# Optimization experiments

Measured on AMD Instinct MI355X. Metric: run time of the kernel, lower is better.

## Reference

```python
import jax, jax.numpy as jnp
import numpy as np

N_TASK, N_WORKER, N_STATION = 20000, 5000, 1000
D, HEADS, LAYERS = 64, 4, 2
EDGE_COUNTS = [50000, 30000, 30000, 40000, 40000]
# (n_src, n_dst) per relation: precedes, assigned_to, has_task, can_do, done_by
EDGE_SPEC = [(N_TASK, N_TASK), (N_TASK, N_STATION), (N_STATION, N_TASK), (N_WORKER, N_TASK), (N_TASK, N_WORKER)]
EDGE_TYPES = [('task', 'task'), ('task', 'station'), ('station', 'task'), ('worker', 'task'), ('task', 'worker')]


def setup_inputs() -> dict:
    key = jax.random.key(0)
    ks = iter(jax.random.split(key, 64))
    inp = {}
    inp['x_task'] = jax.random.normal(next(ks), (N_TASK, 16), jnp.float32)
    inp['x_worker'] = jax.random.normal(next(ks), (N_WORKER, 12), jnp.float32)
    inp['x_station'] = jax.random.normal(next(ks), (N_STATION, 10), jnp.float32)
    for i, (E, (ns, nd)) in enumerate(zip(EDGE_COUNTS, EDGE_SPEC)):
        src = jax.random.randint(next(ks), (E,), 0, ns)
        dst = jax.random.randint(next(ks), (E,), 0, nd)
        inp[f'ei{i}'] = jnp.stack([src, dst]).astype(jnp.int32)
    def lin(k, i, o):
        return jax.random.normal(k, (i, o), jnp.float32) / np.float32(np.sqrt(i))
    # feature embedder params (Linear + LayerNorm affine) per node type
    for name, fd in [('task', 16), ('worker', 12), ('station', 10)]:
        inp[f'W_{name}'] = lin(next(ks), fd, D)
        inp[f'b_{name}'] = jnp.zeros((D,), jnp.float32)
        inp[f'g_{name}'] = jnp.ones((D,), jnp.float32)
        inp[f'beta_{name}'] = jnp.zeros((D,), jnp.float32)
    # stacked GATv2 params: [layers, 5 edge types, ...]
    inp['gat_Wl'] = jax.random.normal(next(ks), (LAYERS, 5, D, HEADS * D), jnp.float32) / np.float32(np.sqrt(D))
    inp['gat_Wr'] = jax.random.normal(next(ks), (LAYERS, 5, D, HEADS * D), jnp.float32) / np.float32(np.sqrt(D))
    inp['gat_att'] = jax.random.normal(next(ks), (LAYERS, 5, HEADS, D), jnp.float32) * np.float32(0.1)
    inp['gat_bias'] = jnp.zeros((LAYERS, 5, D), jnp.float32)
    return inp


def _layer_norm(x, g, b):
    m = x.mean(-1, keepdims=True)
    v = ((x - m) ** 2).mean(-1, keepdims=True)
    return (x - m) * jax.lax.rsqrt(v + 1e-5) * g + b


def _gatv2(x_src, x_dst, ei, Wl, Wr, att, bias):
    # GATv2Conv, concat=False (mean over heads), no self loops
    n_dst = x_dst.shape[0]
    xl = (x_src @ Wl).reshape(-1, HEADS, D)  # [Ns,H,Dh]
    xr = (x_dst @ Wr).reshape(-1, HEADS, D)  # [Nd,H,Dh]
    src, dst = ei[0], ei[1]
    e = jax.nn.leaky_relu(xl[src] + xr[dst], 0.2)          # [E,H,Dh]
    logits = jnp.einsum('ehd,hd->eh', e, att)              # [E,H]
    m = jax.ops.segment_max(logits, dst, num_segments=n_dst)
    ex = jnp.exp(logits - m[dst])
    denom = jax.ops.segment_sum(ex, dst, num_segments=n_dst)
    alpha = ex / denom[dst]                                # segment softmax per dst node
    out = jax.ops.segment_sum(alpha[..., None] * xl[src], dst, num_segments=n_dst)
    return out.mean(axis=1) + bias                         # [Nd,D]


def _forward(x_task, x_worker, x_station, eis,
             W_task, b_task, g_task, beta_task,
             W_worker, b_worker, g_worker, beta_worker,
             W_station, b_station, g_station, beta_station,
             gat_Wl, gat_Wr, gat_att, gat_bias):
    x = {
        'task': jax.nn.relu(_layer_norm(x_task @ W_task + b_task, g_task, beta_task)),
        'worker': jax.nn.relu(_layer_norm(x_worker @ W_worker + b_worker, g_worker, beta_worker)),
        'station': jax.nn.relu(_layer_norm(x_station @ W_station + b_station, g_station, beta_station)),
    }
    for l in range(LAYERS):
        agg = {'task': 0.0, 'worker': 0.0, 'station': 0.0}
        for t, (st, dt) in enumerate(EDGE_TYPES):
            agg[dt] = agg[dt] + _gatv2(x[st], x[dt], eis[t], gat_Wl[l, t], gat_Wr[l, t], gat_att[l, t], gat_bias[l, t])
        x = {k: jax.nn.relu(agg[k]) + x[k] for k in x}  # HeteroConv sum aggr, then ReLU + residual
    gc = jnp.concatenate([
        x['station'].mean(0), x['task'].mean(0), x['worker'].mean(0),
        x['station'].max(0), x['task'].max(0), x['worker'].max(0),
    ])[None, :]  # [1, 6*D]
    return x['task'], x['worker'], x['station'], gc


def reference(x_task, x_worker, x_station, ei0, ei1, ei2, ei3, ei4,
              W_task, b_task, g_task, beta_task,
              W_worker, b_worker, g_worker, beta_worker,
              W_station, b_station, g_station, beta_station,
              gat_Wl, gat_Wr, gat_att, gat_bias):
    return _forward(x_task, x_worker, x_station, (ei0, ei1, ei2, ei3, ei4),
                    W_task, b_task, g_task, beta_task,
                    W_worker, b_worker, g_worker, beta_worker,
                    W_station, b_station, g_station, beta_station,
                    gat_Wl, gat_Wr, gat_att, gat_bias)
```

## Files before the change

### kernel.cpp

```cpp
#include <hip/hip_runtime.h>
#include <math.h>

#define NT 20000
#define NW 5000
#define NS 1000

typedef __attribute__((ext_vector_type(8))) short bf16x8;
typedef __attribute__((ext_vector_type(4))) float f32x4;

struct GemmSeg { const short* X; const short* Wt; short* Y; int N; int blk0; };
struct GemmTab { GemmSeg s[10]; int nseg; };

struct GatSeg { const int* rowp; const int* col; const short* xl; const short* xr;
                const float* att; const float* bias; float* agg; int Nd; int wave0; };
struct GatTab { GatSeg s[5]; int nseg; };

struct EdgeSeg { const int* ei; int* cnt; int* col; int E; int blk0; };
struct EdgeTab { EdgeSeg s[5]; int nseg; };

struct ScanTab { int* cnt[5]; int* rowp[5]; int n[5]; };

__device__ __forceinline__ float wsum64(float v) {
  #pragma unroll
  for (int o = 32; o > 0; o >>= 1) v += __shfl_xor(v, o, 64);
  return v;
}
__device__ __forceinline__ short f2b(float f) {
  unsigned u = __float_as_uint(f);
  unsigned r = (u + 0x7FFFu + ((u >> 16) & 1u)) >> 16;
  return (short)(unsigned short)r;
}
__device__ __forceinline__ float blo(unsigned x) { return __uint_as_float(x << 16); }
__device__ __forceinline__ float bhi(unsigned x) { return __uint_as_float(x & 0xFFFF0000u); }

__global__ void wprep_kernel(const float* __restrict__ gWl, const float* __restrict__ gWr,
                             short* __restrict__ Wlt, short* __restrict__ Wrt,
                             int* __restrict__ nxtAll, int nZero) {
  int idx = blockIdx.x * 256 + threadIdx.x;
  if (idx < nZero) nxtAll[idx] = 0;
  int side = idx >= 163840;
  int j = idx - side * 163840;
  int m = j >> 14;
  int e = j & 16383;
  int k = e >> 8, colv = e & 255;
  const float* src = side ? gWr : gWl;
  short* dst = side ? Wrt : Wlt;
  dst[m * 16384 + colv * 64 + k] = f2b(src[m * 16384 + e]);
}

__global__ void embed_kernel(const float* __restrict__ xT, const float* __restrict__ xW,
                             const float* __restrict__ xS,
                             const float* __restrict__ WT, const float* __restrict__ WW,
                             const float* __restrict__ WS,
                             const float* __restrict__ pT, const float* __restrict__ pW,
                             const float* __restrict__ pS,
                             float* __restrict__ yT, float* __restrict__ yW,
                             float* __restrict__ yS,
                             short* __restrict__ bT, short* __restrict__ bW,
                             short* __restrict__ bS) {
  int gid  = blockIdx.x * blockDim.x + threadIdx.x;
  int wid  = gid >> 6;
  int lane = gid & 63;
  const float* x; const float* W; const float* pp; float* y; short* yb; int FD; int n;
  if (wid < NT)            { x = xT; W = WT; pp = pT; y = yT; yb = bT; FD = 16; n = wid; }
  else if (wid < NT + NW)  { x = xW; W = WW; pp = pW; y = yW; yb = bW; FD = 12; n = wid - NT; }
  else if (wid < NT + NW + NS) { x = xS; W = WS; pp = pS; y = yS; yb = bS; FD = 10; n = wid - NT - NW; }
  else return;
  const float* xr = x + (size_t)n * FD;
  float acc = pp[lane];
  for (int k = 0; k < FD; ++k) acc = fmaf(xr[k], W[k * 64 + lane], acc);
  float m = wsum64(acc) * (1.f / 64.f);
  float d = acc - m;
  float v = wsum64(d * d) * (1.f / 64.f);
  float o = d * rsqrtf(v + 1e-5f) * pp[64 + lane] + pp[128 + lane];
  o = fmaxf(o, 0.f);
  y[(size_t)n * 64 + lane] = o;
  yb[(size_t)n * 64 + lane] = f2b(o);
}

__global__ void packp_kernel(const float* b0, const float* g0, const float* be0,
                             const float* b1, const float* g1, const float* be1,
                             const float* b2, const float* g2, const float* be2,
                             float* __restrict__ out) {
  int i = threadIdx.x;
  out[i]       = b0[i];  out[64 + i]  = g0[i];  out[128 + i] = be0[i];
  out[192 + i] = b1[i];  out[256 + i] = g1[i];  out[320 + i] = be1[i];
  out[384 + i] = b2[i];  out[448 + i] = g2[i];  out[512 + i] = be2[i];
}

__global__ void count_kernel(EdgeTab tab) {
  int b = blockIdx.x, si = 0;
  for (int i = 1; i < tab.nseg; ++i) if (b >= tab.s[i].blk0) si = i;
  EdgeSeg sg = tab.s[si];
  int e = (b - sg.blk0) * 256 + threadIdx.x;
  if (e < sg.E) atomicAdd(&sg.cnt[sg.ei[sg.E + e]], 1);
}

__global__ void scan_kernel(ScanTab tab) {
  int t = blockIdx.x;
  int* cnt = tab.cnt[t]; int* rowp = tab.rowp[t]; int n = tab.n[t];
  __shared__ int wsums[16];
  __shared__ int carry_s;
  int tid = threadIdx.x, lane = tid & 63, w = tid >> 6;
  if (tid == 0) carry_s = 0;
  __syncthreads();
  for (int base = 0; base < n; base += 1024) {
    int i = base + tid;
    int v = (i < n) ? cnt[i] : 0;
    int s = v;
    #pragma unroll
    for (int o = 1; o < 64; o <<= 1) { int x = __shfl_up(s, o, 64); if (lane >= o) s += x; }
    if (lane == 63) wsums[w] = s;
    __syncthreads();
    if (w == 0 && lane < 16) {
      int x = wsums[lane];
      #pragma unroll
      for (int o = 1; o < 16; o <<= 1) { int y = __shfl_up(x, o, 16); if (lane >= o) x += y; }
      wsums[lane] = x;
    }
    __syncthreads();
    int carry   = carry_s;
    int waveoff = (w == 0) ? 0 : wsums[w - 1];
    int exc     = carry + waveoff + s - v;
    if (i < n) { rowp[i] = exc; cnt[i] = exc; }
    __syncthreads();
    if (tid == 0) carry_s += wsums[15];
    __syncthreads();
  }
  if (threadIdx.x == 0) rowp[n] = carry_s;
}

__global__ void fill_kernel(EdgeTab tab) {
  int b = blockIdx.x, si = 0;
  for (int i = 1; i < tab.nseg; ++i) if (b >= tab.s[i].blk0) si = i;
  EdgeSeg sg = tab.s[si];
  int e = (b - sg.blk0) * 256 + threadIdx.x;
  if (e >= sg.E) return;
  int s = sg.ei[e], d = sg.ei[sg.E + e];
  int pos = atomicAdd(&sg.cnt[d], 1);
  sg.col[pos] = s;
}

__global__ __launch_bounds__(256) void gemm_kernel(GemmTab tab) {
  __shared__ short lds[4096 + 16896];
  int b = blockIdx.x, si = 0;
  for (int i = 1; i < tab.nseg; ++i) if (b >= tab.s[i].blk0) si = i;
  GemmSeg sg = tab.s[si];
  int r0 = (b - sg.blk0) * 64;
  int tid = threadIdx.x;
  #pragma unroll
  for (int it = 0; it < 2; ++it) {
    int idx = it * 256 + tid;
    int row = idx >> 3, kq = idx & 7;
    bf16x8 v = {0, 0, 0, 0, 0, 0, 0, 0};
    if (r0 + row < sg.N) v = *(const bf16x8*)&sg.X[(size_t)(r0 + row) * 64 + kq * 8];
    *(bf16x8*)&lds[(row * 8 + (kq ^ (row & 7))) * 8] = v;
  }
  #pragma unroll
  for (int it = 0; it < 8; ++it) {
    int idx = it * 256 + tid;
    int col = idx >> 3, kq = idx & 7;
    bf16x8 v = *(const bf16x8*)&sg.Wt[col * 64 + kq * 8];
    *(bf16x8*)&lds[4096 + (col * 8 + (kq ^ (col & 7))) * 8] = v;
  }
  __syncthreads();
  int lane = tid & 63, wv = tid >> 6;
  int r = lane & 15, hk = lane >> 4;
  f32x4 acc[4][4];
  #pragma unroll
  for (int rt = 0; rt < 4; ++rt)
    #pragma unroll
    for (int ct = 0; ct < 4; ++ct) acc[rt][ct] = (f32x4){0.f, 0.f, 0.f, 0.f};
  #pragma unroll
  for (int kk = 0; kk < 2; ++kk) {
    int kq = kk * 4 + hk;
    bf16x8 a[4], bb[4];
    #pragma unroll
    for (int rt = 0; rt < 4; ++rt) {
      int row = rt * 16 + r;
      a[rt] = *(const bf16x8*)&lds[(row * 8 + (kq ^ (row & 7))) * 8];
    }
    #pragma unroll
    for (int ct = 0; ct < 4; ++ct) {
      int col = wv * 64 + ct * 16 + r;
      bb[ct] = *(const bf16x8*)&lds[4096 + (col * 8 + (kq ^ (col & 7))) * 8];
    }
    #pragma unroll
    for (int rt = 0; rt < 4; ++rt)
      #pragma unroll
      for (int ct = 0; ct < 4; ++ct)
        acc[rt][ct] = __builtin_amdgcn_mfma_f32_16x16x32_bf16(a[rt], bb[ct], acc[rt][ct], 0, 0, 0);
  }
  __syncthreads();
  #pragma unroll
  for (int rt = 0; rt < 4; ++rt)
    #pragma unroll
    for (int j = 0; j < 4; ++j) {
      int rowl = rt * 16 + hk * 4 + j;
      #pragma unroll
      for (int ct = 0; ct < 4; ++ct)
        lds[rowl * 264 + wv * 64 + ct * 16 + r] = f2b(acc[rt][ct][j]);
    }
  __syncthreads();
  #pragma unroll
  for (int it = 0; it < 8; ++it) {
    int idx = it * 256 + tid;
    int row = idx >> 5, v8 = idx & 31;
    if (r0 + row < sg.N) {
      bf16x8 v = *(const bf16x8*)&lds[row * 264 + v8 * 8];
      *(bf16x8*)&sg.Y[(size_t)(r0 + row) * 256 + v8 * 8] = v;
    }
  }
}

__global__ void gat_kernel(GatTab tab) {
  int gwave = (blockIdx.x * blockDim.x + threadIdx.x) >> 6;
  int lane  = threadIdx.x & 63;
  int si = 0;
  for (int i = 1; i < tab.nseg; ++i) if (gwave >= tab.s[i].wave0) si = i;
  GatSeg sg = tab.s[si];
  int n = gwave - sg.wave0;
  if (n >= sg.Nd) return;
  int h = lane >> 4, lig = lane & 15;
  uint2 xru = *(const uint2*)&sg.xr[(size_t)n * 256 + h * 64 + lig * 4];
  float4 a4 = *(const float4*)&sg.att[h * 64 + lig * 4];
  int beg = sg.rowp[n], end = sg.rowp[n + 1];
  int d = end - beg;
  float xr0 = blo(xru.x), xr1 = bhi(xru.x), xr2 = blo(xru.y), xr3 = bhi(xru.y);
  float den = 0.f, c0 = 0.f, c1 = 0.f, c2 = 0.f, c3 = 0.f;
  for (int sc = 0; sc < d; sc += 64) {
    int scn = min(64, d - sc);
    int myc = (lane < scn) ? sg.col[beg + sc + lane] : 0;
    for (int cb = 0; cb < scn; cb += 8) {
      int m = min(8, scn - cb);
      uint2 w[8];
      #pragma unroll
      for (int k = 0; k < 8; ++k)
        if (k < m) {
          int c = __shfl(myc, cb + k, 64);
          w[k] = *(const uint2*)&sg.xl[(size_t)c * 256 + h * 64 + lig * 4];
        }
      #pragma unroll
      for (int k = 0; k < 8; ++k)
        if (k < m) {
          float f0 = blo(w[k].x), f1 = bhi(w[k].x), f2v = blo(w[k].y), f3 = bhi(w[k].y);
          float vx = f0 + xr0, vy = f1 + xr1, vz = f2v + xr2, vw = f3 + xr3;
          vx = fmaxf(vx, 0.2f * vx); vy = fmaxf(vy, 0.2f * vy);
          vz = fmaxf(vz, 0.2f * vz); vw = fmaxf(vw, 0.2f * vw);
          float dd = fmaf(vx, a4.x, fmaf(vy, a4.y, fmaf(vz, a4.z, vw * a4.w)));
          dd += __shfl_xor(dd, 1, 64);
          dd += __shfl_xor(dd, 2, 64);
          dd += __shfl_xor(dd, 4, 64);
          dd += __shfl_xor(dd, 8, 64);
          float e = __expf(dd);
          den += e;
          c0 = fmaf(e, f0, c0); c1 = fmaf(e, f1, c1);
          c2 = fmaf(e, f2v, c2); c3 = fmaf(e, f3, c3);
        }
    }
  }
  float4 o = make_float4(0.f, 0.f, 0.f, 0.f);
  if (d > 0) {
    float inv = 1.f / den;
    o.x = c0 * inv; o.y = c1 * inv; o.z = c2 * inv; o.w = c3 * inv;
  }
  o.x += __shfl_xor(o.x, 16, 64); o.x += __shfl_xor(o.x, 32, 64);
  o.y += __shfl_xor(o.y, 16, 64); o.y += __shfl_xor(o.y, 32, 64);
  o.z += __shfl_xor(o.z, 16, 64); o.z += __shfl_xor(o.z, 32, 64);
  o.w += __shfl_xor(o.w, 16, 64); o.w += __shfl_xor(o.w, 32, 64);
  if (lane < 16) {
    float4 b4 = *(const float4*)&sg.bias[lane * 4];
    float4 res;
    res.x = fmaf(0.25f, o.x, b4.x); res.y = fmaf(0.25f, o.y, b4.y);
    res.z = fmaf(0.25f, o.z, b4.z); res.w = fmaf(0.25f, o.w, b4.w);
    *(float4*)&sg.agg[(size_t)n * 64 + lane * 4] = res;
  }
}

__global__ void combine_kernel(const float4* __restrict__ aT0, const float4* __restrict__ aT2,
                               const float4* __restrict__ aT3, const float4* __restrict__ aW,
                               const float4* __restrict__ aS,
                               const float4* __restrict__ xT, const float4* __restrict__ xW,
                               const float4* __restrict__ xS,
                               float4* __restrict__ oT, float4* __restrict__ oW,
                               float4* __restrict__ oS,
                               unsigned* __restrict__ bT, unsigned* __restrict__ bW,
                               unsigned* __restrict__ bS) {
  int i = blockIdx.x * 256 + threadIdx.x;
  const int nT4 = NT * 16, nW4 = NW * 16, nS4 = NS * 16;
  const float4* a; const float4* x; float4* o; unsigned* bo; int j; bool sum3 = false;
  const float4 *a2 = nullptr, *a3 = nullptr;
  if (i < nT4)                 { a = aT0; a2 = aT2; a3 = aT3; x = xT; o = oT; bo = bT; j = i; sum3 = true; }
  else if (i < nT4 + nW4)      { a = aW; x = xW; o = oW; bo = bW; j = i - nT4; }
  else if (i < nT4 + nW4 + nS4){ a = aS; x = xS; o = oS; bo = bS; j = i - nT4 - nW4; }
  else return;
  float4 av = a[j];
  if (sum3) {
    float4 v2 = a2[j], v3 = a3[j];
    av.x += v2.x + v3.x; av.y += v2.y + v3.y; av.z += v2.z + v3.z; av.w += v2.w + v3.w;
  }
  float4 xv = x[j];
  float4 r;
  r.x = fmaxf(av.x, 0.f) + xv.x; r.y = fmaxf(av.y, 0.f) + xv.y;
  r.z = fmaxf(av.z, 0.f) + xv.z; r.w = fmaxf(av.w, 0.f) + xv.w;
  o[j] = r;
  if (bo) {
    unsigned lo = (unsigned)(unsigned short)f2b(r.x) | ((unsigned)(unsigned short)f2b(r.y) << 16);
    unsigned hi = (unsigned)(unsigned short)f2b(r.z) | ((unsigned)(unsigned short)f2b(r.w) << 16);
    bo[j * 2] = lo; bo[j * 2 + 1] = hi;
  }
}

__global__ __launch_bounds__(256) void pool1_kernel(const float* __restrict__ xt,
                                                    const float* __restrict__ xw,
                                                    const float* __restrict__ xs,
                                                    float* __restrict__ part_sum,
                                                    float* __restrict__ part_max) {
  int b = blockIdx.x;
  const float* x; int N, base, nb;
  if (b < 80)       { x = xt; N = NT; base = 0;   nb = 80; }
  else if (b < 100) { x = xw; N = NW; base = 80;  nb = 20; }
  else              { x = xs; N = NS; base = 100; nb = 4;  }
  int local = b - base;
  int lane = threadIdx.x & 63, w = threadIdx.x >> 6;
  int waveIdx = local * 4 + w, stride = nb * 4;
  float s = 0.f, mx = -3e38f;
  for (int r = waveIdx; r < N; r += stride) {
    float v = x[(size_t)r * 64 + lane];
    s += v; mx = fmaxf(mx, v);
  }
  __shared__ float ss[4][64], sm[4][64];
  ss[w][lane] = s; sm[w][lane] = mx;
  __syncthreads();
  if (w == 0) {
    #pragma unroll
    for (int i = 1; i < 4; ++i) { s += ss[i][lane]; mx = fmaxf(mx, sm[i][lane]); }
    part_sum[(size_t)b * 64 + lane] = s;
    part_max[(size_t)b * 64 + lane] = mx;
  }
}

__global__ void pool2_kernel(const float* __restrict__ part_sum,
                             const float* __restrict__ part_max,
                             float* __restrict__ gc) {
  int b = blockIdx.x;
  int lane = threadIdx.x & 63, w = threadIdx.x >> 6;
  int off, cnt, N, mi;
  if (b == 0)      { off = 100; cnt = 4;  N = NS; mi = 0;   }
  else if (b == 1) { off = 0;   cnt = 80; N = NT; mi = 64;  }
  else             { off = 80;  cnt = 20; N = NW; mi = 128; }
  float s = 0.f, mx = -3e38f;
  for (int i = w; i < cnt; i += 4) {
    s += part_sum[(size_t)(off + i) * 64 + lane];
    mx = fmaxf(mx, part_max[(size_t)(off + i) * 64 + lane]);
  }
  __shared__ float ss[4][64], sm[4][64];
  ss[w][lane] = s; sm[w][lane] = mx;
  __syncthreads();
  if (w == 0) {
    #pragma unroll
    for (int i = 1; i < 4; ++i) { s += ss[i][lane]; mx = fmaxf(mx, sm[i][lane]); }
    gc[mi + lane] = s / (float)N;
    gc[192 + mi + lane] = mx;
  }
}

extern "C" void kernel_launch(void* const* d_in, const int* in_sizes, int n_in,
                              void* d_out, int out_size, void* d_ws, size_t ws_size,
                              hipStream_t stream) {
  const float* x_in[3] = {(const float*)d_in[0], (const float*)d_in[1], (const float*)d_in[2]};
  const int*   ei[5]   = {(const int*)d_in[3], (const int*)d_in[4], (const int*)d_in[5],
                          (const int*)d_in[6], (const int*)d_in[7]};
  const float* Wemb[3] = {(const float*)d_in[8],  (const float*)d_in[12], (const float*)d_in[16]};
  const float* bemb[3] = {(const float*)d_in[9],  (const float*)d_in[13], (const float*)d_in[17]};
  const float* gemb[3] = {(const float*)d_in[10], (const float*)d_in[14], (const float*)d_in[18]};
  const float* beemb[3]= {(const float*)d_in[11], (const float*)d_in[15], (const float*)d_in[19]};
  const float* gWl   = (const float*)d_in[20];
  const float* gWr   = (const float*)d_in[21];
  const float* gatt  = (const float*)d_in[22];
  const float* gbias = (const float*)d_in[23];

  const int NN[3]  = {NT, NW, NS};
  const int EC[5]  = {50000, 30000, 30000, 40000, 40000};
  const int STy[5] = {0, 0, 2, 1, 0};
  const int DTy[5] = {0, 2, 0, 0, 1};

  char* p = (char*)d_ws;
  auto alloc = [&](size_t bytes) -> void* {
    void* r = (void*)p;
    p += (bytes + 255) & ~(size_t)255;
    return r;
  };
  float* xc[3];  short* xcb[3];
  for (int k = 0; k < 3; ++k) xc[k]  = (float*)alloc((size_t)NN[k] * 64 * 4);
  for (int k = 0; k < 3; ++k) xcb[k] = (short*)alloc((size_t)NN[k] * 64 * 2);
  float* aggT0 = (float*)alloc((size_t)NT * 64 * 4);
  float* aggS  = (float*)alloc((size_t)NS * 64 * 4);
  float* aggT2 = (float*)alloc((size_t)NT * 64 * 4);
  float* aggT3 = (float*)alloc((size_t)NT * 64 * 4);
  float* aggW  = (float*)alloc((size_t)NW * 64 * 4);
  float* aggOf[5] = {aggT0, aggS, aggT2, aggT3, aggW};
  int* nxtAll = (int*)alloc((size_t)66000 * 4);
  int  nxtOff[5] = {0, NT, NT + NS, 2 * NT + NS, 3 * NT + NS};
  int* nxt[5]; for (int t = 0; t < 5; ++t) nxt[t] = nxtAll + nxtOff[t];
  int *rowp[5], *col[5];
  for (int t = 0; t < 5; ++t) {
    rowp[t] = (int*)alloc((size_t)(NN[DTy[t]] + 1) * 4);
    col[t]  = (int*)alloc((size_t)EC[t] * 4);
  }
  float* psum = (float*)alloc((size_t)104 * 64 * 4);
  float* pmax = (float*)alloc((size_t)104 * 64 * 4);
  short* Wlt  = (short*)alloc((size_t)10 * 16384 * 2);
  short* Wrt  = (short*)alloc((size_t)10 * 16384 * 2);
  float* ppk  = (float*)alloc((size_t)576 * 4);

  size_t used = (size_t)(p - (char*)d_ws);
  size_t fusedExtra = (size_t)132000 * 256 * 2 + (1 << 20);
  bool fused = (ws_size - used) >= fusedExtra;
  short *xlT[5], *xrT[5];
  if (fused) {
    for (int t = 0; t < 5; ++t) {
      xlT[t] = (short*)alloc((size_t)NN[STy[t]] * 256 * 2);
      xrT[t] = (short*)alloc((size_t)NN[DTy[t]] * 256 * 2);
    }
  } else {
    short* xlb = (short*)alloc((size_t)NT * 256 * 2);
    short* xrb = (short*)alloc((size_t)NT * 256 * 2);
    for (int t = 0; t < 5; ++t) { xlT[t] = xlb; xrT[t] = xrb; }
  }

  wprep_kernel<<<1280, 256, 0, stream>>>(gWl, gWr, Wlt, Wrt, nxtAll, 66000);
  packp_kernel<<<1, 64, 0, stream>>>(bemb[0], gemb[0], beemb[0],
                                     bemb[1], gemb[1], beemb[1],
                                     bemb[2], gemb[2], beemb[2], ppk);

  embed_kernel<<<(26000 * 64 + 255) / 256, 256, 0, stream>>>(
      x_in[0], x_in[1], x_in[2], Wemb[0], Wemb[1], Wemb[2],
      ppk, ppk + 192, ppk + 384,
      xc[0], xc[1], xc[2], xcb[0], xcb[1], xcb[2]);

  EdgeTab etab; etab.nseg = 5;
  int eb = 0;
  for (int t = 0; t < 5; ++t) {
    etab.s[t] = {ei[t], nxt[t], col[t], EC[t], eb};
    eb += (EC[t] + 255) / 256;
  }
  count_kernel<<<eb, 256, 0, stream>>>(etab);
  ScanTab stab;
  for (int t = 0; t < 5; ++t) { stab.cnt[t] = nxt[t]; stab.rowp[t] = rowp[t]; stab.n[t] = NN[DTy[t]]; }
  scan_kernel<<<5, 1024, 0, stream>>>(stab);
  fill_kernel<<<eb, 256, 0, stream>>>(etab);

  float* outT = (float*)d_out;
  float* outW = outT + (size_t)NT * 64;
  float* outS = outW + (size_t)NW * 64;
  float* gc   = outS + (size_t)NS * 64;

  for (int l = 0; l < 2; ++l) {
    if (fused) {
      GemmTab gt; gt.nseg = 10;
      int gb = 0;
      for (int t = 0; t < 5; ++t) {
        size_t off = (size_t)(l * 5 + t);
        gt.s[2 * t + 0] = {xcb[STy[t]], Wlt + off * 16384, xlT[t], NN[STy[t]], gb};
        gb += (NN[STy[t]] + 63) / 64;
        gt.s[2 * t + 1] = {xcb[DTy[t]], Wrt + off * 16384, xrT[t], NN[DTy[t]], gb};
        gb += (NN[DTy[t]] + 63) / 64;
      }
      gemm_kernel<<<gb, 256, 0, stream>>>(gt);

      GatTab at; at.nseg = 5;
      int wv = 0;
      for (int t = 0; t < 5; ++t) {
        size_t off = (size_t)(l * 5 + t);
        at.s[t] = {rowp[t], col[t], xlT[t], xrT[t], gatt + off * 256, gbias + off * 64,
                   aggOf[t], NN[DTy[t]], wv};
        wv += NN[DTy[t]];
      }
      gat_kernel<<<(wv * 64 + 255) / 256, 256, 0, stream>>>(at);
    } else {
      for (int t = 0; t < 5; ++t) {
        size_t off = (size_t)(l * 5 + t);
        GemmTab gt; gt.nseg = 2;
        gt.s[0] = {xcb[STy[t]], Wlt + off * 16384, xlT[t], NN[STy[t]], 0};
        int gb = (NN[STy[t]] + 63) / 64;
        gt.s[1] = {xcb[DTy[t]], Wrt + off * 16384, xrT[t], NN[DTy[t]], gb};
        gb += (NN[DTy[t]] + 63) / 64;
        gemm_kernel<<<gb, 256, 0, stream>>>(gt);
        GatTab at; at.nseg = 1;
        at.s[0] = {rowp[t], col[t], xlT[t], xrT[t], gatt + off * 256, gbias + off * 64,
                   aggOf[t], NN[DTy[t]], 0};
        gat_kernel<<<((NN[DTy[t]] + 3) / 4), 256, 0, stream>>>(at);
      }
    }
    float* dT = (l == 1) ? outT : xc[0];
    float* dW = (l == 1) ? outW : xc[1];
    float* dS = (l == 1) ? outS : xc[2];
    unsigned* bT = (l == 1) ? nullptr : (unsigned*)xcb[0];
    unsigned* bW = (l == 1) ? nullptr : (unsigned*)xcb[1];
    unsigned* bS = (l == 1) ? nullptr : (unsigned*)xcb[2];
    combine_kernel<<<(26000 * 16 + 255) / 256, 256, 0, stream>>>(
        (const float4*)aggT0, (const float4*)aggT2, (const float4*)aggT3,
        (const float4*)aggW, (const float4*)aggS,
        (const float4*)xc[0], (const float4*)xc[1], (const float4*)xc[2],
        (float4*)dT, (float4*)dW, (float4*)dS, bT, bW, bS);
  }

  pool1_kernel<<<104, 256, 0, stream>>>(outT, outW, outS, psum, pmax);
  pool2_kernel<<<3, 256, 0, stream>>>(psum, pmax, gc);
}
```

Before: 253.9 us.

## Fuse prep kernels, merge per-destination GAT relations, fold pooling into combine

Merges weight prep, param packing and embedding into one launch. The GAT kernel now handles all incoming relations per destination node in one wave, summing results directly instead of writing three separate task aggregates. It also walks edges serially with a one-ahead prefetch in place of the 8-wide batched gather. The final combine computes per-block partial sum and max for pooling, which removes the separate pool1 pass, and the non-fused fallback path is dropped. Fewer launches and less aggregate traffic are traded for more serial gather latency and a larger final reduction in pool2.

```diff
diff --git a/kernel.cpp b/kernel.cpp
--- a/kernel.cpp
+++ b/kernel.cpp
@@ -8,17 +8,32 @@
 typedef __attribute__((ext_vector_type(8))) short bf16x8;
 typedef __attribute__((ext_vector_type(4))) float f32x4;
 
+#define CB_T 1250
+#define CB_W 313
+#define CB_S 63
+#define CB_ALL 1626
+
 struct GemmSeg { const short* X; const short* Wt; short* Y; int N; int blk0; };
 struct GemmTab { GemmSeg s[10]; int nseg; };
 
-struct GatSeg { const int* rowp; const int* col; const short* xl; const short* xr;
-                const float* att; const float* bias; float* agg; int Nd; int wave0; };
-struct GatTab { GatSeg s[5]; int nseg; };
+struct GatTab {
+  const int* rowp[5]; const int* col[5];
+  const short* xl[5]; const short* xr[5];
+  const float* att; const float* bias;
+  float* aggT; float* aggW; float* aggS;
+};
 
 struct EdgeSeg { const int* ei; int* cnt; int* col; int E; int blk0; };
 struct EdgeTab { EdgeSeg s[5]; int nseg; };
 
 struct ScanTab { int* cnt[5]; int* rowp[5]; int n[5]; };
+
+struct Mega0 {
+  const float *xT, *xW, *xS, *WT, *WW, *WS;
+  const float *bT, *gT, *beT, *bW, *gW, *beW, *bS, *gS, *beS;
+  float *yT, *yW, *yS; short *ybT, *ybW, *ybS;
+  const float *gWl, *gWr; short *Wlt, *Wrt; int* nxtAll;
+};
 
 __device__ __forceinline__ float wsum64(float v) {
   #pragma unroll
@@ -33,59 +48,36 @@
 __device__ __forceinline__ float blo(unsigned x) { return __uint_as_float(x << 16); }
 __device__ __forceinline__ float bhi(unsigned x) { return __uint_as_float(x & 0xFFFF0000u); }
 
-__global__ void wprep_kernel(const float* __restrict__ gWl, const float* __restrict__ gWr,
-                             short* __restrict__ Wlt, short* __restrict__ Wrt,
-                             int* __restrict__ nxtAll, int nZero) {
-  int idx = blockIdx.x * 256 + threadIdx.x;
-  if (idx < nZero) nxtAll[idx] = 0;
-  int side = idx >= 163840;
-  int j = idx - side * 163840;
-  int m = j >> 14;
-  int e = j & 16383;
-  int k = e >> 8, colv = e & 255;
-  const float* src = side ? gWr : gWl;
-  short* dst = side ? Wrt : Wlt;
-  dst[m * 16384 + colv * 64 + k] = f2b(src[m * 16384 + e]);
-}
-
-__global__ void embed_kernel(const float* __restrict__ xT, const float* __restrict__ xW,
-                             const float* __restrict__ xS,
-                             const float* __restrict__ WT, const float* __restrict__ WW,
-                             const float* __restrict__ WS,
-                             const float* __restrict__ pT, const float* __restrict__ pW,
-                             const float* __restrict__ pS,
-                             float* __restrict__ yT, float* __restrict__ yW,
-                             float* __restrict__ yS,
-                             short* __restrict__ bT, short* __restrict__ bW,
-                             short* __restrict__ bS) {
-  int gid  = blockIdx.x * blockDim.x + threadIdx.x;
-  int wid  = gid >> 6;
-  int lane = gid & 63;
-  const float* x; const float* W; const float* pp; float* y; short* yb; int FD; int n;
-  if (wid < NT)            { x = xT; W = WT; pp = pT; y = yT; yb = bT; FD = 16; n = wid; }
-  else if (wid < NT + NW)  { x = xW; W = WW; pp = pW; y = yW; yb = bW; FD = 12; n = wid - NT; }
-  else if (wid < NT + NW + NS) { x = xS; W = WS; pp = pS; y = yS; yb = bS; FD = 10; n = wid - NT - NW; }
-  else return;
-  const float* xr = x + (size_t)n * FD;
-  float acc = pp[lane];
-  for (int k = 0; k < FD; ++k) acc = fmaf(xr[k], W[k * 64 + lane], acc);
-  float m = wsum64(acc) * (1.f / 64.f);
-  float d = acc - m;
-  float v = wsum64(d * d) * (1.f / 64.f);
-  float o = d * rsqrtf(v + 1e-5f) * pp[64 + lane] + pp[128 + lane];
-  o = fmaxf(o, 0.f);
-  y[(size_t)n * 64 + lane] = o;
-  yb[(size_t)n * 64 + lane] = f2b(o);
-}
-
-__global__ void packp_kernel(const float* b0, const float* g0, const float* be0,
-                             const float* b1, const float* g1, const float* be1,
-                             const float* b2, const float* g2, const float* be2,
-                             float* __restrict__ out) {
-  int i = threadIdx.x;
-  out[i]       = b0[i];  out[64 + i]  = g0[i];  out[128 + i] = be0[i];
-  out[192 + i] = b1[i];  out[256 + i] = g1[i];  out[320 + i] = be1[i];
-  out[384 + i] = b2[i];  out[448 + i] = g2[i];  out[512 + i] = be2[i];
+__global__ void mega0_kernel(Mega0 M) {
+  int b = blockIdx.x;
+  if (b < 6500) {
+    int gid = b * 256 + threadIdx.x;
+    int wid = gid >> 6, lane = gid & 63;
+    const float *x, *W, *bb, *gg, *be; float* y; short* yb; int FD, n;
+    if (wid < NT)            { x = M.xT; W = M.WT; bb = M.bT; gg = M.gT; be = M.beT; y = M.yT; yb = M.ybT; FD = 16; n = wid; }
+    else if (wid < NT + NW)  { x = M.xW; W = M.WW; bb = M.bW; gg = M.gW; be = M.beW; y = M.yW; yb = M.ybW; FD = 12; n = wid - NT; }
+    else                     { x = M.xS; W = M.WS; bb = M.bS; gg = M.gS; be = M.beS; y = M.yS; yb = M.ybS; FD = 10; n = wid - NT - NW; }
+    const float* xr = x + (size_t)n * FD;
+    float acc = bb[lane];
+    for (int k = 0; k < FD; ++k) acc = fmaf(xr[k], W[k * 64 + lane], acc);
+    float m = wsum64(acc) * (1.f / 64.f);
+    float d = acc - m;
+    float v = wsum64(d * d) * (1.f / 64.f);
+    float o = d * rsqrtf(v + 1e-5f) * gg[lane] + be[lane];
+    o = fmaxf(o, 0.f);
+    y[(size_t)n * 64 + lane] = o;
+    yb[(size_t)n * 64 + lane] = f2b(o);
+  } else {
+    int idx = (b - 6500) * 256 + threadIdx.x;
+    if (idx < 66000) M.nxtAll[idx] = 0;
+    int side = idx >= 163840;
+    int j = idx - side * 163840;
+    int m = j >> 14, e = j & 16383;
+    int k = e >> 8, colv = e & 255;
+    const float* src = side ? M.gWr : M.gWl;
+    short* dst = side ? M.Wrt : M.Wlt;
+    dst[m * 16384 + colv * 64 + k] = f2b(src[m * 16384 + e]);
+  }
 }
 
 __global__ void count_kernel(EdgeTab tab) {
@@ -216,150 +208,142 @@
 __global__ void gat_kernel(GatTab tab) {
   int gwave = (blockIdx.x * blockDim.x + threadIdx.x) >> 6;
   int lane  = threadIdx.x & 63;
-  int si = 0;
-  for (int i = 1; i < tab.nseg; ++i) if (gwave >= tab.s[i].wave0) si = i;
-  GatSeg sg = tab.s[si];
-  int n = gwave - sg.wave0;
-  if (n >= sg.Nd) return;
   int h = lane >> 4, lig = lane & 15;
-  uint2 xru = *(const uint2*)&sg.xr[(size_t)n * 256 + h * 64 + lig * 4];
-  float4 a4 = *(const float4*)&sg.att[h * 64 + lig * 4];
-  int beg = sg.rowp[n], end = sg.rowp[n + 1];
-  int d = end - beg;
-  float xr0 = blo(xru.x), xr1 = bhi(xru.x), xr2 = blo(xru.y), xr3 = bhi(xru.y);
-  float den = 0.f, c0 = 0.f, c1 = 0.f, c2 = 0.f, c3 = 0.f;
-  for (int sc = 0; sc < d; sc += 64) {
-    int scn = min(64, d - sc);
-    int myc = (lane < scn) ? sg.col[beg + sc + lane] : 0;
-    for (int cb = 0; cb < scn; cb += 8) {
-      int m = min(8, scn - cb);
-      uint2 w[8];
+  int nrel, n; float* agg;
+  int rels[3];
+  if (gwave < NT)            { nrel = 3; rels[0] = 0; rels[1] = 2; rels[2] = 3; n = gwave; agg = tab.aggT; }
+  else if (gwave < NT + NW)  { nrel = 1; rels[0] = 4; rels[1] = 4; rels[2] = 4; n = gwave - NT; agg = tab.aggW; }
+  else if (gwave < NT + NW + NS) { nrel = 1; rels[0] = 1; rels[1] = 1; rels[2] = 1; n = gwave - NT - NW; agg = tab.aggS; }
+  else return;
+  float o0 = 0.f, o1 = 0.f, o2 = 0.f, o3 = 0.f;
+  for (int ri = 0; ri < nrel; ++ri) {
+    int r = rels[ri];
+    int beg = tab.rowp[r][n], end = tab.rowp[r][n + 1];
+    const short* xl = tab.xl[r];
+    const int* colp = tab.col[r];
+    uint2 xru = *(const uint2*)&tab.xr[r][(size_t)n * 256 + h * 64 + lig * 4];
+    float4 a4 = *(const float4*)&tab.att[r * 256 + h * 64 + lig * 4];
+    float xr0 = blo(xru.x), xr1 = bhi(xru.x), xr2 = blo(xru.y), xr3 = bhi(xru.y);
+    if (end > beg) {
+      float den = 0.f, c0 = 0.f, c1 = 0.f, c2 = 0.f, c3 = 0.f;
+      int sNxt = colp[beg];
+      uint2 w = *(const uint2*)&xl[(size_t)sNxt * 256 + h * 64 + lig * 4];
+      if (beg + 1 < end) sNxt = colp[beg + 1];
+      for (int i = beg; i < end; ++i) {
+        uint2 wc = w;
+        if (i + 1 < end) w = *(const uint2*)&xl[(size_t)sNxt * 256 + h * 64 + lig * 4];
+        if (i + 2 < end) sNxt = colp[i + 2];
+        float f0 = blo(wc.x), f1 = bhi(wc.x), f2v = blo(wc.y), f3 = bhi(wc.y);
+        float vx = f0 + xr0, vy = f1 + xr1, vz = f2v + xr2, vw = f3 + xr3;
+        vx = fmaxf(vx, 0.2f * vx); vy = fmaxf(vy, 0.2f * vy);
+        vz = fmaxf(vz, 0.2f * vz); vw = fmaxf(vw, 0.2f * vw);
+        float dd = fmaf(vx, a4.x, fmaf(vy, a4.y, fmaf(vz, a4.z, vw * a4.w)));
+        dd += __shfl_xor(dd, 1, 64);
+        dd += __shfl_xor(dd, 2, 64);
+        dd += __shfl_xor(dd, 4, 64);
+        dd += __shfl_xor(dd, 8, 64);
+        float e = __expf(dd);
+        den += e;
+        c0 = fmaf(e, f0, c0); c1 = fmaf(e, f1, c1);
+        c2 = fmaf(e, f2v, c2); c3 = fmaf(e, f3, c3);
+      }
+      float inv = 1.f / den;
+      o0 = fmaf(c0, inv, o0); o1 = fmaf(c1, inv, o1);
+      o2 = fmaf(c2, inv, o2); o3 = fmaf(c3, inv, o3);
+    }
+  }
+  o0 += __shfl_xor(o0, 16, 64); o0 += __shfl_xor(o0, 32, 64);
+  o1 += __shfl_xor(o1, 16, 64); o1 += __shfl_xor(o1, 32, 64);
+  o2 += __shfl_xor(o2, 16, 64); o2 += __shfl_xor(o2, 32, 64);
+  o3 += __shfl_xor(o3, 16, 64); o3 += __shfl_xor(o3, 32, 64);
+  if (lane < 16) {
+    float4 bs = make_float4(0.f, 0.f, 0.f, 0.f);
+    for (int ri = 0; ri < nrel; ++ri) {
+      float4 b4 = *(const float4*)&tab.bias[rels[ri] * 64 + lane * 4];
+      bs.x += b4.x; bs.y += b4.y; bs.z += b4.z; bs.w += b4.w;
+    }
+    float4 res;
+    res.x = fmaf(0.25f, o0, bs.x); res.y = fmaf(0.25f, o1, bs.y);
+    res.z = fmaf(0.25f, o2, bs.z); res.w = fmaf(0.25f, o3, bs.w);
+    *(float4*)&agg[(size_t)n * 64 + lane * 4] = res;
+  }
+}
+
+template <int POOL>
+__global__ __launch_bounds__(256) void combine_kernel(
+    const float4* __restrict__ aT, const float4* __restrict__ aW, const float4* __restrict__ aS,
+    const float4* __restrict__ xT, const float4* __restrict__ xW, const float4* __restrict__ xS,
+    float4* __restrict__ oT, float4* __restrict__ oW, float4* __restrict__ oS,
+    unsigned* __restrict__ bT, unsigned* __restrict__ bW, unsigned* __restrict__ bS,
+    float4* __restrict__ psum, float4* __restrict__ pmax) {
+  int b = blockIdx.x, tid = threadIdx.x;
+  const float4 *a, *x; float4* o; unsigned* bo; int n4, local;
+  if (b < CB_T)              { a = aT; x = xT; o = oT; bo = bT; n4 = NT * 16; local = b; }
+  else if (b < CB_T + CB_W)  { a = aW; x = xW; o = oW; bo = bW; n4 = NW * 16; local = b - CB_T; }
+  else                       { a = aS; x = xS; o = oS; bo = bS; n4 = NS * 16; local = b - CB_T - CB_W; }
+  int j = local * 256 + tid;
+  bool valid = j < n4;
+  float4 r = make_float4(0.f, 0.f, 0.f, 0.f);
+  if (valid) {
+    float4 av = a[j], xv = x[j];
+    r.x = fmaxf(av.x, 0.f) + xv.x; r.y = fmaxf(av.y, 0.f) + xv.y;
+    r.z = fmaxf(av.z, 0.f) + xv.z; r.w = fmaxf(av.w, 0.f) + xv.w;
+    o[j] = r;
+    if (POOL == 0 && bo) {
+      unsigned lo = (unsigned)(unsigned short)f2b(r.x) | ((unsigned)(unsigned short)f2b(r.y) << 16);
+      unsigned hi = (unsigned)(unsigned short)f2b(r.z) | ((unsigned)(unsigned short)f2b(r.w) << 16);
+      bo[j * 2] = lo; bo[j * 2 + 1] = hi;
+    }
+  }
+  if (POOL) {
+    float4 s = r;
+    float4 m = valid ? r : make_float4(-3e38f, -3e38f, -3e38f, -3e38f);
+    #pragma unroll
+    for (int off = 16; off <= 32; off <<= 1) {
+      s.x += __shfl_xor(s.x, off, 64); s.y += __shfl_xor(s.y, off, 64);
+      s.z += __shfl_xor(s.z, off, 64); s.w += __shfl_xor(s.w, off, 64);
+      m.x = fmaxf(m.x, __shfl_xor(m.x, off, 64)); m.y = fmaxf(m.y, __shfl_xor(m.y, off, 64));
+      m.z = fmaxf(m.z, __shfl_xor(m.z, off, 64)); m.w = fmaxf(m.w, __shfl_xor(m.w, off, 64));
+    }
+    __shared__ float4 ls[4][16], lm[4][16];
+    int w = tid >> 6, q = tid & 15;
+    if (((tid >> 4) & 3) == 0) { ls[w][q] = s; lm[w][q] = m; }
+    __syncthreads();
+    if (tid < 16) {
+      float4 S = ls[0][tid], M = lm[0][tid];
       #pragma unroll
-      for (int k = 0; k < 8; ++k)
-        if (k < m) {
-          int c = __shfl(myc, cb + k, 64);
-          w[k] = *(const uint2*)&sg.xl[(size_t)c * 256 + h * 64 + lig * 4];
-        }
-      #pragma unroll
-      for (int k = 0; k < 8; ++k)
-        if (k < m) {
-          float f0 = blo(w[k].x), f1 = bhi(w[k].x), f2v = blo(w[k].y), f3 = bhi(w[k].y);
-          float vx = f0 + xr0, vy = f1 + xr1, vz = f2v + xr2, vw = f3 + xr3;
-          vx = fmaxf(vx, 0.2f * vx); vy = fmaxf(vy, 0.2f * vy);
-          vz = fmaxf(vz, 0.2f * vz); vw = fmaxf(vw, 0.2f * vw);
-          float dd = fmaf(vx, a4.x, fmaf(vy, a4.y, fmaf(vz, a4.z, vw * a4.w)));
-          dd += __shfl_xor(dd, 1, 64);
-          dd += __shfl_xor(dd, 2, 64);
-          dd += __shfl_xor(dd, 4, 64);
-          dd += __shfl_xor(dd, 8, 64);
-          float e = __expf(dd);
-          den += e;
-          c0 = fmaf(e, f0, c0); c1 = fmaf(e, f1, c1);
-          c2 = fmaf(e, f2v, c2); c3 = fmaf(e, f3, c3);
-        }
-    }
-  }
-  float4 o = make_float4(0.f, 0.f, 0.f, 0.f);
-  if (d > 0) {
-    float inv = 1.f / den;
-    o.x = c0 * inv; o.y = c1 * inv; o.z = c2 * inv; o.w = c3 * inv;
-  }
-  o.x += __shfl_xor(o.x, 16, 64); o.x += __shfl_xor(o.x, 32, 64);
-  o.y += __shfl_xor(o.y, 16, 64); o.y += __shfl_xor(o.y, 32, 64);
-  o.z += __shfl_xor(o.z, 16, 64); o.z += __shfl_xor(o.z, 32, 64);
-  o.w += __shfl_xor(o.w, 16, 64); o.w += __shfl_xor(o.w, 32, 64);
-  if (lane < 16) {
-    float4 b4 = *(const float4*)&sg.bias[lane * 4];
-    float4 res;
-    res.x = fmaf(0.25f, o.x, b4.x); res.y = fmaf(0.25f, o.y, b4.y);
-    res.z = fmaf(0.25f, o.z, b4.z); res.w = fmaf(0.25f, o.w, b4.w);
-    *(float4*)&sg.agg[(size_t)n * 64 + lane * 4] = res;
-  }
-}
-
-__global__ void combine_kernel(const float4* __restrict__ aT0, const float4* __restrict__ aT2,
-                               const float4* __restrict__ aT3, const float4* __restrict__ aW,
-                               const float4* __restrict__ aS,
-                               const float4* __restrict__ xT, const float4* __restrict__ xW,
-                               const float4* __restrict__ xS,
-                               float4* __restrict__ oT, float4* __restrict__ oW,
-                               float4* __restrict__ oS,
-                               unsigned* __restrict__ bT, unsigned* __restrict__ bW,
-                               unsigned* __restrict__ bS) {
-  int i = blockIdx.x * 256 + threadIdx.x;
-  const int nT4 = NT * 16, nW4 = NW * 16, nS4 = NS * 16;
-  const float4* a; const float4* x; float4* o; unsigned* bo; int j; bool sum3 = false;
-  const float4 *a2 = nullptr, *a3 = nullptr;
-  if (i < nT4)                 { a = aT0; a2 = aT2; a3 = aT3; x = xT; o = oT; bo = bT; j = i; sum3 = true; }
-  else if (i < nT4 + nW4)      { a = aW; x = xW; o = oW; bo = bW; j = i - nT4; }
-  else if (i < nT4 + nW4 + nS4){ a = aS; x = xS; o = oS; bo = bS; j = i - nT4 - nW4; }
-  else return;
-  float4 av = a[j];
-  if (sum3) {
-    float4 v2 = a2[j], v3 = a3[j];
-    av.x += v2.x + v3.x; av.y += v2.y + v3.y; av.z += v2.z + v3.z; av.w += v2.w + v3.w;
-  }
-  float4 xv = x[j];
-  float4 r;
-  r.x = fmaxf(av.x, 0.f) + xv.x; r.y = fmaxf(av.y, 0.f) + xv.y;
-  r.z = fmaxf(av.z, 0.f) + xv.z; r.w = fmaxf(av.w, 0.f) + xv.w;
-  o[j] = r;
-  if (bo) {
-    unsigned lo = (unsigned)(unsigned short)f2b(r.x) | ((unsigned)(unsigned short)f2b(r.y) << 16);
-    unsigned hi = (unsigned)(unsigned short)f2b(r.z) | ((unsigned)(unsigned short)f2b(r.w) << 16);
-    bo[j * 2] = lo; bo[j * 2 + 1] = hi;
-  }
-}
-
-__global__ __launch_bounds__(256) void pool1_kernel(const float* __restrict__ xt,
-                                                    const float* __restrict__ xw,
-                                                    const float* __restrict__ xs,
-                                                    float* __restrict__ part_sum,
-                                                    float* __restrict__ part_max) {
-  int b = blockIdx.x;
-  const float* x; int N, base, nb;
-  if (b < 80)       { x = xt; N = NT; base = 0;   nb = 80; }
-  else if (b < 100) { x = xw; N = NW; base = 80;  nb = 20; }
-  else              { x = xs; N = NS; base = 100; nb = 4;  }
-  int local = b - base;
-  int lane = threadIdx.x & 63, w = threadIdx.x >> 6;
-  int waveIdx = local * 4 + w, stride = nb * 4;
-  float s = 0.f, mx = -3e38f;
-  for (int r = waveIdx; r < N; r += stride) {
-    float v = x[(size_t)r * 64 + lane];
-    s += v; mx = fmaxf(mx, v);
-  }
-  __shared__ float ss[4][64], sm[4][64];
-  ss[w][lane] = s; sm[w][lane] = mx;
-  __syncthreads();
-  if (w == 0) {
-    #pragma unroll
-    for (int i = 1; i < 4; ++i) { s += ss[i][lane]; mx = fmaxf(mx, sm[i][lane]); }
-    part_sum[(size_t)b * 64 + lane] = s;
-    part_max[(size_t)b * 64 + lane] = mx;
-  }
-}
-
-__global__ void pool2_kernel(const float* __restrict__ part_sum,
-                             const float* __restrict__ part_max,
+      for (int i = 1; i < 4; ++i) {
+        float4 s2 = ls[i][tid], m2 = lm[i][tid];
+        S.x += s2.x; S.y += s2.y; S.z += s2.z; S.w += s2.w;
+        M.x = fmaxf(M.x, m2.x); M.y = fmaxf(M.y, m2.y);
+        M.z = fmaxf(M.z, m2.z); M.w = fmaxf(M.w, m2.w);
+      }
+      psum[b * 16 + tid] = S;
+      pmax[b * 16 + tid] = M;
+    }
+  }
+}
+
+__global__ void pool2_kernel(const float* __restrict__ psum,
+                             const float* __restrict__ pmax,
                              float* __restrict__ gc) {
   int b = blockIdx.x;
   int lane = threadIdx.x & 63, w = threadIdx.x >> 6;
   int off, cnt, N, mi;
-  if (b == 0)      { off = 100; cnt = 4;  N = NS; mi = 0;   }
-  else if (b == 1) { off = 0;   cnt = 80; N = NT; mi = 64;  }
-  else             { off = 80;  cnt = 20; N = NW; mi = 128; }
+  if (b == 0)      { off = CB_T + CB_W; cnt = CB_S; N = NS; mi = 0;   }
+  else if (b == 1) { off = 0;           cnt = CB_T; N = NT; mi = 64;  }
+  else             { off = CB_T;        cnt = CB_W; N = NW; mi = 128; }
   float s = 0.f, mx = -3e38f;
-  for (int i = w; i < cnt; i += 4) {
-    s += part_sum[(size_t)(off + i) * 64 + lane];
-    mx = fmaxf(mx, part_max[(size_t)(off + i) * 64 + lane]);
-  }
-  __shared__ float ss[4][64], sm[4][64];
+  for (int i = w; i < cnt; i += 16) {
+    s += psum[(size_t)(off + i) * 64 + lane];
+    mx = fmaxf(mx, pmax[(size_t)(off + i) * 64 + lane]);
+  }
+  __shared__ float ss[16][64], sm[16][64];
   ss[w][lane] = s; sm[w][lane] = mx;
   __syncthreads();
   if (w == 0) {
     #pragma unroll
-    for (int i = 1; i < 4; ++i) { s += ss[i][lane]; mx = fmaxf(mx, sm[i][lane]); }
+    for (int i = 1; i < 16; ++i) { s += ss[i][lane]; mx = fmaxf(mx, sm[i][lane]); }
     gc[mi + lane] = s / (float)N;
     gc[192 + mi + lane] = mx;
   }
@@ -394,12 +378,9 @@
   float* xc[3];  short* xcb[3];
   for (int k = 0; k < 3; ++k) xc[k]  = (float*)alloc((size_t)NN[k] * 64 * 4);
   for (int k = 0; k < 3; ++k) xcb[k] = (short*)alloc((size_t)NN[k] * 64 * 2);
-  float* aggT0 = (float*)alloc((size_t)NT * 64 * 4);
-  float* aggS  = (float*)alloc((size_t)NS * 64 * 4);
-  float* aggT2 = (float*)alloc((size_t)NT * 64 * 4);
-  float* aggT3 = (float*)alloc((size_t)NT * 64 * 4);
-  float* aggW  = (float*)alloc((size_t)NW * 64 * 4);
-  float* aggOf[5] = {aggT0, aggS, aggT2, aggT3, aggW};
+  float* aggT = (float*)alloc((size_t)NT * 64 * 4);
+  float* aggW = (float*)alloc((size_t)NW * 64 * 4);
+  float* aggS = (float*)alloc((size_t)NS * 64 * 4);
   int* nxtAll = (int*)alloc((size_t)66000 * 4);
   int  nxtOff[5] = {0, NT, NT + NS, 2 * NT + NS, 3 * NT + NS};
   int* nxt[5]; for (int t = 0; t < 5; ++t) nxt[t] = nxtAll + nxtOff[t];
@@ -408,36 +389,15 @@
     rowp[t] = (int*)alloc((size_t)(NN[DTy[t]] + 1) * 4);
     col[t]  = (int*)alloc((size_t)EC[t] * 4);
   }
-  float* psum = (float*)alloc((size_t)104 * 64 * 4);
-  float* pmax = (float*)alloc((size_t)104 * 64 * 4);
+  float* psum = (float*)alloc((size_t)CB_ALL * 64 * 4);
+  float* pmax = (float*)alloc((size_t)CB_ALL * 64 * 4);
   short* Wlt  = (short*)alloc((size_t)10 * 16384 * 2);
   short* Wrt  = (short*)alloc((size_t)10 * 16384 * 2);
-  float* ppk  = (float*)alloc((size_t)576 * 4);
-
-  size_t used = (size_t)(p - (char*)d_ws);
-  size_t fusedExtra = (size_t)132000 * 256 * 2 + (1 << 20);
-  bool fused = (ws_size - used) >= fusedExtra;
   short *xlT[5], *xrT[5];
-  if (fused) {
-    for (int t = 0; t < 5; ++t) {
-      xlT[t] = (short*)alloc((size_t)NN[STy[t]] * 256 * 2);
-      xrT[t] = (short*)alloc((size_t)NN[DTy[t]] * 256 * 2);
-    }
-  } else {
-    short* xlb = (short*)alloc((size_t)NT * 256 * 2);
-    short* xrb = (short*)alloc((size_t)NT * 256 * 2);
-    for (int t = 0; t < 5; ++t) { xlT[t] = xlb; xrT[t] = xrb; }
-  }
-
-  wprep_kernel<<<1280, 256, 0, stream>>>(gWl, gWr, Wlt, Wrt, nxtAll, 66000);
-  packp_kernel<<<1, 64, 0, stream>>>(bemb[0], gemb[0], beemb[0],
-                                     bemb[1], gemb[1], beemb[1],
-                                     bemb[2], gemb[2], beemb[2], ppk);
-
-  embed_kernel<<<(26000 * 64 + 255) / 256, 256, 0, stream>>>(
-      x_in[0], x_in[1], x_in[2], Wemb[0], Wemb[1], Wemb[2],
-      ppk, ppk + 192, ppk + 384,
-      xc[0], xc[1], xc[2], xcb[0], xcb[1], xcb[2]);
+  for (int t = 0; t < 5; ++t) {
+    xlT[t] = (short*)alloc((size_t)NN[STy[t]] * 256 * 2);
+    xrT[t] = (short*)alloc((size_t)NN[DTy[t]] * 256 * 2);
+  }
 
   EdgeTab etab; etab.nseg = 5;
   int eb = 0;
@@ -445,6 +405,18 @@
     etab.s[t] = {ei[t], nxt[t], col[t], EC[t], eb};
     eb += (EC[t] + 255) / 256;
   }
+
+  Mega0 M;
+  M.xT = x_in[0]; M.xW = x_in[1]; M.xS = x_in[2];
+  M.WT = Wemb[0]; M.WW = Wemb[1]; M.WS = Wemb[2];
+  M.bT = bemb[0]; M.gT = gemb[0]; M.beT = beemb[0];
+  M.bW = bemb[1]; M.gW = gemb[1]; M.beW = beemb[1];
+  M.bS = bemb[2]; M.gS = gemb[2]; M.beS = beemb[2];
+  M.yT = xc[0]; M.yW = xc[1]; M.yS = xc[2];
+  M.ybT = xcb[0]; M.ybW = xcb[1]; M.ybS = xcb[2];
+  M.gWl = gWl; M.gWr = gWr; M.Wlt = Wlt; M.Wrt = Wrt; M.nxtAll = nxtAll;
+  mega0_kernel<<<7780, 256, 0, stream>>>(M);
+
   count_kernel<<<eb, 256, 0, stream>>>(etab);
   ScanTab stab;
   for (int t = 0; t < 5; ++t) { stab.cnt[t] = nxt[t]; stab.rowp[t] = rowp[t]; stab.n[t] = NN[DTy[t]]; }
@@ -457,55 +429,43 @@
   float* gc   = outS + (size_t)NS * 64;
 
   for (int l = 0; l < 2; ++l) {
-    if (fused) {
-      GemmTab gt; gt.nseg = 10;
-      int gb = 0;
-      for (int t = 0; t < 5; ++t) {
-        size_t off = (size_t)(l * 5 + t);
-        gt.s[2 * t + 0] = {xcb[STy[t]], Wlt + off * 16384, xlT[t], NN[STy[t]], gb};
-        gb += (NN[STy[t]] + 63) / 64;
-        gt.s[2 * t + 1] = {xcb[DTy[t]], Wrt + off * 16384, xrT[t], NN[DTy[t]], gb};
-        gb += (NN[DTy[t]] + 63) / 64;
-      }
-      gemm_kernel<<<gb, 256, 0, stream>>>(gt);
-
-      GatTab at; at.nseg = 5;
-      int wv = 0;
-      for (int t = 0; t < 5; ++t) {
-        size_t off = (size_t)(l * 5 + t);
-        at.s[t] = {rowp[t], col[t], xlT[t], xrT[t], gatt + off * 256, gbias + off * 64,
-                   aggOf[t], NN[DTy[t]], wv};
-        wv += NN[DTy[t]];
-      }
-      gat_kernel<<<(wv * 64 + 255) / 256, 256, 0, stream>>>(at);
+    GemmTab gt; gt.nseg = 10;
+    int gb = 0;
+    for (int t = 0; t < 5; ++t) {
+      size_t off = (size_t)(l * 5 + t);
+      gt.s[2 * t + 0] = {xcb[STy[t]], Wlt + off * 16384, xlT[t], NN[STy[t]], gb};
+      gb += (NN[STy[t]] + 63) / 64;
+      gt.s[2 * t + 1] = {xcb[DTy[t]], Wrt + off * 16384, xrT[t], NN[DTy[t]], gb};
+      gb += (NN[DTy[t]] + 63) / 64;
+    }
+    gemm_kernel<<<gb, 256, 0, stream>>>(gt);
+
+    GatTab at;
+    for (int t = 0; t < 5; ++t) {
+      at.rowp[t] = rowp[t]; at.col[t] = col[t];
+      at.xl[t] = xlT[t]; at.xr[t] = xrT[t];
+    }
+    at.att  = gatt  + (size_t)l * 5 * 256;
+    at.bias = gbias + (size_t)l * 5 * 64;
+    at.aggT = aggT; at.aggW = aggW; at.aggS = aggS;
+    gat_kernel<<<(26000 * 64 + 255) / 256, 256, 0, stream>>>(at);
+
+    if (l == 0) {
+      combine_kernel<0><<<CB_ALL, 256, 0, stream>>>(
+          (const float4*)aggT, (const float4*)aggW, (const float4*)aggS,
+          (const float4*)xc[0], (const float4*)xc[1], (const float4*)xc[2],
+          (float4*)xc[0], (float4*)xc[1], (float4*)xc[2],
+          (unsigned*)xcb[0], (unsigned*)xcb[1], (unsigned*)xcb[2],
+          nullptr, nullptr);
     } else {
-      for (int t = 0; t < 5; ++t) {
-        size_t off = (size_t)(l * 5 + t);
-        GemmTab gt; gt.nseg = 2;
-        gt.s[0] = {xcb[STy[t]], Wlt + off * 16384, xlT[t], NN[STy[t]], 0};
-        int gb = (NN[STy[t]] + 63) / 64;
-        gt.s[1] = {xcb[DTy[t]], Wrt + off * 16384, xrT[t], NN[DTy[t]], gb};
-        gb += (NN[DTy[t]] + 63) / 64;
-        gemm_kernel<<<gb, 256, 0, stream>>>(gt);
-        GatTab at; at.nseg = 1;
-        at.s[0] = {rowp[t], col[t], xlT[t], xrT[t], gatt + off * 256, gbias + off * 64,
-                   aggOf[t], NN[DTy[t]], 0};
-        gat_kernel<<<((NN[DTy[t]] + 3) / 4), 256, 0, stream>>>(at);
-      }
-    }
-    float* dT = (l == 1) ? outT : xc[0];
-    float* dW = (l == 1) ? outW : xc[1];
-    float* dS = (l == 1) ? outS : xc[2];
-    unsigned* bT = (l == 1) ? nullptr : (unsigned*)xcb[0];
-    unsigned* bW = (l == 1) ? nullptr : (unsigned*)xcb[1];
-    unsigned* bS = (l == 1) ? nullptr : (unsigned*)xcb[2];
-    combine_kernel<<<(26000 * 16 + 255) / 256, 256, 0, stream>>>(
-        (const float4*)aggT0, (const float4*)aggT2, (const float4*)aggT3,
-        (const float4*)aggW, (const float4*)aggS,
-        (const float4*)xc[0], (const float4*)xc[1], (const float4*)xc[2],
-        (float4*)dT, (float4*)dW, (float4*)dS, bT, bW, bS);
-  }
-
-  pool1_kernel<<<104, 256, 0, stream>>>(outT, outW, outS, psum, pmax);
-  pool2_kernel<<<3, 256, 0, stream>>>(psum, pmax, gc);
-}
+      combine_kernel<1><<<CB_ALL, 256, 0, stream>>>(
+          (const float4*)aggT, (const float4*)aggW, (const float4*)aggS,
+          (const float4*)xc[0], (const float4*)xc[1], (const float4*)xc[2],
+          (float4*)outT, (float4*)outW, (float4*)outS,
+          nullptr, nullptr, nullptr,
+          (float4*)psum, (float4*)pmax);
+    }
+  }
+
+  pool2_kernel<<<3, 1024, 0, stream>>>(psum, pmax, gc);
+}
```

Measured after the change: 236.0 us. 7.1% less time.
